# Kernel optimization log

Measured on AMD Instinct MI355X. Metric: run time of the kernel, lower is better.

## Reference

```python
import jax, jax.numpy as jnp
import numpy as np

B, L, H, NH, NB = 16, 256, 64, 2, 2
HS = H // NH
MAXLEN, TIME_SPAN, ITEMNUM = 256, 256, 50000
NEG = -4294967295.0  # -2**32 + 1
EPS = 1e-8


def layernorm(x, g, b):
    m = jnp.mean(x, axis=-1, keepdims=True)
    v = jnp.mean((x - m) ** 2, axis=-1, keepdims=True)
    return g * (x - m) / jnp.sqrt(v + EPS) + b


def setup_inputs() -> dict:
    key = jax.random.key(0)
    ks = jax.random.split(key, 24)
    s = 0.02
    inp = {
        "seqs_data": jax.random.randint(ks[0], (B, L), 0, ITEMNUM, dtype=jnp.int32),
        "seqs": jax.random.normal(ks[1], (B, L, H), dtype=jnp.float32),
        "positions": jax.random.randint(ks[2], (B, L), 0, MAXLEN, dtype=jnp.int32),
        "time_matrices": jax.random.randint(ks[3], (B, L, L), 0, TIME_SPAN + 1, dtype=jnp.int32),
        "abs_pos_K_tab": jax.random.normal(ks[4], (MAXLEN, H)) * s,
        "abs_pos_V_tab": jax.random.normal(ks[5], (MAXLEN, H)) * s,
        "time_K_tab": jax.random.normal(ks[6], (TIME_SPAN + 1, H)) * s,
        "time_V_tab": jax.random.normal(ks[7], (TIME_SPAN + 1, H)) * s,
        "Qw": jax.random.normal(ks[8], (NB, H, H)) * s,
        "Qb": jnp.zeros((NB, H)),
        "Kw": jax.random.normal(ks[9], (NB, H, H)) * s,
        "Kb": jnp.zeros((NB, H)),
        "Vw": jax.random.normal(ks[10], (NB, H, H)) * s,
        "Vb": jnp.zeros((NB, H)),
        "ln1_g": jnp.ones((NB, H)), "ln1_b": jnp.zeros((NB, H)),
        "ln2_g": jnp.ones((NB, H)), "ln2_b": jnp.zeros((NB, H)),
        "ffn_W1": jax.random.normal(ks[11], (NB, H, H)) * s,
        "ffn_b1": jnp.zeros((NB, H)),
        "ffn_W2": jax.random.normal(ks[12], (NB, H, H)) * s,
        "ffn_b2": jnp.zeros((NB, H)),
        "last_g": jnp.ones((H,)), "last_b": jnp.zeros((H,)),
    }
    return inp


def _forward(seqs_data, seqs, positions, time_matrices,
             abs_pos_K_tab, abs_pos_V_tab, time_K_tab, time_V_tab,
             Qw, Qb, Kw, Kb, Vw, Vb, ln1_g, ln1_b, ln2_g, ln2_b,
             ffn_W1, ffn_b1, ffn_W2, ffn_b2, last_g, last_b):
    # abs-pos embeddings with padding_idx=0 (zero row, no grad flow to it)
    pos_keep = (positions != 0)[..., None].astype(seqs.dtype)
    abs_pos_K = abs_pos_K_tab[positions] * pos_keep            # [B,L,H]
    abs_pos_V = abs_pos_V_tab[positions] * pos_keep
    time_K = time_K_tab[time_matrices]                         # [B,L,L,H]
    time_V = time_V_tab[time_matrices]
    tmK = time_K.reshape(B, L, L, NH, HS)
    tmV = time_V.reshape(B, L, L, NH, HS)
    aK = abs_pos_K.reshape(B, L, NH, HS)
    aV = abs_pos_V.reshape(B, L, NH, HS)

    timeline_mask = (seqs_data == ITEMNUM - 1)                 # [B,L] True = pad
    keep = (~timeline_mask)[..., None].astype(seqs.dtype)
    seqs = seqs * keep
    causal = ~jnp.tril(jnp.ones((L, L), dtype=bool))           # [L,L] upper tri
    full_mask = timeline_mask[:, None, :, None] | causal[None, None]  # [B,1,L,L]

    for i in range(NB):
        q_in = layernorm(seqs, ln1_g[i], ln1_b[i])
        Q = (q_in @ Qw[i].T + Qb[i]).reshape(B, L, NH, HS)
        K = (seqs @ Kw[i].T + Kb[i]).reshape(B, L, NH, HS)
        V = (seqs @ Vw[i].T + Vb[i]).reshape(B, L, NH, HS)
        aw = (jnp.einsum('blhd,bmhd->bhlm', Q, K)
              + jnp.einsum('blhd,bmhd->bhlm', Q, aK)
              + jnp.einsum('blmhd,blhd->bhlm', tmK, Q)) / (HS ** 0.5)
        aw = jnp.where(full_mask, NEG, aw)
        A = jax.nn.softmax(aw, axis=-1)                        # [B,NH,L,L]
        out = (jnp.einsum('bhlm,bmhd->blhd', A, V)
               + jnp.einsum('bhlm,bmhd->blhd', A, aV)
               + jnp.einsum('bhlm,blmhd->blhd', A, tmV)).reshape(B, L, H)
        seqs = q_in + out
        seqs = layernorm(seqs, ln2_g[i], ln2_b[i])
        h = jax.nn.relu(seqs @ ffn_W1[i].T + ffn_b1[i])
        seqs = (h @ ffn_W2[i].T + ffn_b2[i]) + seqs
        seqs = seqs * keep
    return layernorm(seqs, last_g, last_b)


def reference(seqs_data, seqs, positions, time_matrices,
              abs_pos_K_tab, abs_pos_V_tab, time_K_tab, time_V_tab,
              Qw, Qb, Kw, Kb, Vw, Vb, ln1_g, ln1_b, ln2_g, ln2_b,
              ffn_W1, ffn_b1, ffn_W2, ffn_b2, last_g, last_b):
    return _forward(seqs_data, seqs, positions, time_matrices,
                    abs_pos_K_tab, abs_pos_V_tab, time_K_tab, time_V_tab,
                    Qw, Qb, Kw, Kb, Vw, Vb, ln1_g, ln1_b, ln2_g, ln2_b,
                    ffn_W1, ffn_b1, ffn_W2, ffn_b2, last_g, last_b)
```

## Files before the change

### kernel.cpp

```cpp
#include <hip/hip_runtime.h>
#include <math.h>

#define BATCH 16
#define SEQL  256
#define HDIM  64
#define NBLK  2
#define PADID 49999
#define NEGV  -4294967295.0f
#define LNEPS 1e-8f
#define INV_SQRT_HS 0.17677669529663687f
#define TKC   257
#define TKTLD 260
#define QG    4

__device__ __forceinline__ float waveReduceSum(float v) {
#pragma unroll
    for (int o = 32; o > 0; o >>= 1) v += __shfl_xor(v, o);
    return v;
}

__global__ __launch_bounds__(256) void setup_kernel(
    const float* __restrict__ Qw, const float* __restrict__ Kw,
    const float* __restrict__ Vw, const float* __restrict__ W1,
    const float* __restrict__ W2, const float* __restrict__ tKtab,
    float* __restrict__ QwT, float* __restrict__ KwT, float* __restrict__ VwT,
    float* __restrict__ W1T, float* __restrict__ W2T, float* __restrict__ tKtabT)
{
    __shared__ float tile[64][65];
    const int tid = threadIdx.x;
    const int blk = blockIdx.x;
    if (blk < 10) {
        const float* srcs[10] = {Qw, Qw+4096, Kw, Kw+4096, Vw, Vw+4096,
                                 W1, W1+4096, W2, W2+4096};
        float*       dsts[10] = {QwT, QwT+4096, KwT, KwT+4096, VwT, VwT+4096,
                                 W1T, W1T+4096, W2T, W2T+4096};
        const float* s = srcs[blk];
        float*       d = dsts[blk];
        for (int p = 0; p < 16; ++p) {
            int r = p*4 + (tid>>6), c = tid&63;
            tile[r][c] = s[r*64 + c];
        }
        __syncthreads();
        for (int p = 0; p < 16; ++p) {
            int mth = p*4 + (tid>>6), t = tid&63;
            d[mth*64 + t] = tile[t][mth];
        }
    } else {
        const int s0 = (blk - 10) * 64;
        const int nrows = min(64, TKC - s0);
        for (int p = 0; p < 16; ++p) {
            int rr = p*4 + (tid>>6), c = tid&63;
            if (rr < nrows) tile[rr][c] = tKtab[(size_t)(s0+rr)*64 + c];
        }
        __syncthreads();
        for (int p = 0; p < 16; ++p) {
            int dd = p*4 + (tid>>6), cc = tid&63;
            if (cc < nrows) tKtabT[dd*TKTLD + s0 + cc] = tile[cc][dd];
        }
    }
}

__global__ __launch_bounds__(256) void prep_kernel(
    const float* __restrict__ xin, const int* __restrict__ seqs_data,
    const int* __restrict__ positions,
    const float* __restrict__ QwT, const float* __restrict__ Qb,
    const float* __restrict__ KwT, const float* __restrict__ Kb,
    const float* __restrict__ VwT, const float* __restrict__ Vb,
    const float* __restrict__ g1, const float* __restrict__ b1,
    const float* __restrict__ apK, const float* __restrict__ apV,
    float* __restrict__ q_in, float* __restrict__ Qo,
    float* __restrict__ KpT, float* __restrict__ Vp)
{
    const int w = threadIdx.x >> 6;
    const int t = threadIdx.x & 63;
    const int row0 = blockIdx.x * 4;
    const int row = row0 + w;
    float x = xin[(size_t)row * HDIM + t];
    if (seqs_data[row] == PADID) x = 0.f;

    float mean = waveReduceSum(x) * (1.f / HDIM);
    float d = x - mean;
    float var = waveReduceSum(d * d) * (1.f / HDIM);
    float q = g1[t] * d / sqrtf(var + LNEPS) + b1[t];

    __shared__ float xs[4][HDIM];
    __shared__ float qs[4][HDIM];
    __shared__ float kx[HDIM][5];
    xs[w][t] = x; qs[w][t] = q;
    q_in[(size_t)row * HDIM + t] = q;

    int pos = positions[row];
    float aK = pos ? apK[(size_t)pos * HDIM + t] : 0.f;
    float aV = pos ? apV[(size_t)pos * HDIM + t] : 0.f;

    float aq = 0.f, ak = 0.f, av = 0.f;
#pragma unroll 16
    for (int mth = 0; mth < 64; ++mth) {
        float qm = qs[w][mth], xm = xs[w][mth];
        aq += qm * QwT[mth*64 + t];
        ak += xm * KwT[mth*64 + t];
        av += xm * VwT[mth*64 + t];
    }
    Qo[(size_t)row * HDIM + t] = aq + Qb[t];
    Vp[(size_t)row * HDIM + t] = av + Vb[t] + aV;
    kx[t][w] = ak + Kb[t] + aK;
    __syncthreads();
    const int f = threadIdx.x >> 2, j = threadIdx.x & 3;
    KpT[(size_t)f * 4096 + row0 + j] = kx[f][j];
}

__global__ __launch_bounds__(512) void attn_kernel(
    const float* __restrict__ Qo, const float* __restrict__ KpT,
    const float* __restrict__ Vp, const float* __restrict__ q_in,
    const int* __restrict__ seqs_data, const int* __restrict__ tmat,
    const float* __restrict__ tVtab, const float* __restrict__ tKtabT,
    float* __restrict__ x2)
{
    const int hw  = blockIdx.x;
    const int blk = (hw & 7) * 128 + (hw >> 3);
    const int b   = blk >> 6;
    const int l0  = (blk & 63) << 2;
    const int row0 = b * SEQL + l0;
    const int tid = threadIdx.x;
    const int m   = tid & 255;
    const int h   = tid >> 8;
    const int lane = tid & 63;
    const int wv  = tid >> 6;
    const int mw  = wv & 3;

    __shared__ float qs_l[QG][HDIM];
    __shared__ float Tk_l[QG][2][TKTLD];
    __shared__ float A_s[QG][2][SEQL];
    __shared__ float Wl[QG][2][TKTLD];
    __shared__ float outred[8][QG][HDIM];
    __shared__ float redm[QG][2][4];
    __shared__ float reds[QG][2][4];

    for (int k = tid; k < QG*2*TKTLD; k += 512) ((float*)Wl)[k] = 0.f;
    if (tid < QG*HDIM)
        qs_l[tid >> 6][tid & 63] = Qo[(size_t)(row0 + (tid >> 6)) * HDIM + (tid & 63)];

    bool qpad[QG]; bool anypad = false;
#pragma unroll
    for (int li = 0; li < QG; ++li) {
        qpad[li] = (seqs_data[row0 + li] == PADID);
        anypad |= qpad[li];
    }
    const int lmax = l0 + QG - 1;
    int tmc[QG];
#pragma unroll
    for (int li = 0; li < QG; ++li)
        tmc[li] = tmat[(size_t)(row0 + li) * SEQL + m];
    __syncthreads();

    if (tid < TKC) {
        const int c = tid;
        float a00=0.f,a10=0.f,a20=0.f,a30=0.f, a01=0.f,a11=0.f,a21=0.f,a31=0.f;
#pragma unroll 8
        for (int dd = 0; dd < 32; ++dd) {
            float tt = tKtabT[dd*TKTLD + c];
            a00 += tt * qs_l[0][dd]; a10 += tt * qs_l[1][dd];
            a20 += tt * qs_l[2][dd]; a30 += tt * qs_l[3][dd];
        }
#pragma unroll 8
        for (int dd = 32; dd < 64; ++dd) {
            float tt = tKtabT[dd*TKTLD + c];
            a01 += tt * qs_l[0][dd]; a11 += tt * qs_l[1][dd];
            a21 += tt * qs_l[2][dd]; a31 += tt * qs_l[3][dd];
        }
        Tk_l[0][0][c]=a00; Tk_l[1][0][c]=a10; Tk_l[2][0][c]=a20; Tk_l[3][0][c]=a30;
        Tk_l[0][1][c]=a01; Tk_l[1][1][c]=a11; Tk_l[2][1][c]=a21; Tk_l[3][1][c]=a31;
    }
    __syncthreads();

    float sv[QG];
    const bool waveAllMasked = (mw * 64 > lmax) && !anypad;
    if (waveAllMasked) {
#pragma unroll
        for (int li = 0; li < QG; ++li) sv[li] = NEGV;
    } else {
        float s0=0.f, s1=0.f, s2=0.f, s3=0.f;
        const float* kpb = KpT + (size_t)(h*32) * 4096 + (size_t)b * SEQL + m;
        const float* q0 = &qs_l[0][h*32];
        const float* q1 = &qs_l[1][h*32];
        const float* q2 = &qs_l[2][h*32];
        const float* q3 = &qs_l[3][h*32];
#pragma unroll 8
        for (int dd = 0; dd < 32; ++dd) {
            float kv = kpb[(size_t)dd * 4096];
            s0 += kv * q0[dd]; s1 += kv * q1[dd];
            s2 += kv * q2[dd]; s3 += kv * q3[dd];
        }
        float sarr[QG] = {s0, s1, s2, s3};
#pragma unroll
        for (int li = 0; li < QG; ++li) {
            float s = (sarr[li] + Tk_l[li][h][tmc[li]]) * INV_SQRT_HS;
            const bool masked = (m > l0 + li) || qpad[li];
            sv[li] = masked ? NEGV : s;
        }
    }
#pragma unroll
    for (int li = 0; li < QG; ++li) {
        float a = sv[li];
#pragma unroll
        for (int o = 32; o > 0; o >>= 1) a = fmaxf(a, __shfl_xor(a, o));
        if (lane == 0) redm[li][h][mw] = a;
    }
    __syncthreads();
#pragma unroll
    for (int li = 0; li < QG; ++li) {
        float mx = fmaxf(fmaxf(redm[li][h][0], redm[li][h][1]),
                         fmaxf(redm[li][h][2], redm[li][h][3]));
        float e = __expf(sv[li] - mx);
        sv[li] = e;
        float t = waveReduceSum(e);
        if (lane == 0) reds[li][h][mw] = t;
    }
    __syncthreads();
#pragma unroll
    for (int li = 0; li < QG; ++li) {
        float sum = reds[li][h][0] + reds[li][h][1] + reds[li][h][2] + reds[li][h][3];
        float a = sv[li] / sum;
        A_s[li][h][m] = a;
        if (a != 0.f) atomicAdd(&Wl[li][h][tmc[li]], a);
    }
    __syncthreads();

    const int hd = tid & 63, chunk = tid >> 6;
    const int hh = hd >> 5;
    float acc0 = 0.f, acc1 = 0.f, acc2 = 0.f, acc3 = 0.f;

    const int mend = anypad ? SEQL : (lmax + 1 < SEQL ? lmax + 1 : SEQL);
    const float* vpb = Vp + (size_t)(b * SEQL) * HDIM + hd;
    int mm = chunk;
    for (; mm + 8 < mend; mm += 16) {
        float v0 = vpb[(size_t)(mm)   * HDIM];
        float v1 = vpb[(size_t)(mm+8) * HDIM];
        acc0 += A_s[0][hh][mm]*v0 + A_s[0][hh][mm+8]*v1;
        acc1 += A_s[1][hh][mm]*v0 + A_s[1][hh][mm+8]*v1;
        acc2 += A_s[2][hh][mm]*v0 + A_s[2][hh][mm+8]*v1;
        acc3 += A_s[3][hh][mm]*v0 + A_s[3][hh][mm+8]*v1;
    }
    for (; mm < mend; mm += 8) {
        float vp = vpb[(size_t)mm * HDIM];
        acc0 += A_s[0][hh][mm]*vp; acc1 += A_s[1][hh][mm]*vp;
        acc2 += A_s[2][hh][mm]*vp; acc3 += A_s[3][hh][mm]*vp;
    }
    const float* tvb = tVtab + hd;
    int c = chunk;
    for (; c + 8 < TKC; c += 16) {
        float t0 = tvb[(size_t)(c)   * HDIM];
        float t1 = tvb[(size_t)(c+8) * HDIM];
        acc0 += Wl[0][hh][c]*t0 + Wl[0][hh][c+8]*t1;
        acc1 += Wl[1][hh][c]*t0 + Wl[1][hh][c+8]*t1;
        acc2 += Wl[2][hh][c]*t0 + Wl[2][hh][c+8]*t1;
        acc3 += Wl[3][hh][c]*t0 + Wl[3][hh][c+8]*t1;
    }
    for (; c < TKC; c += 8) {
        float tv = tvb[(size_t)c * HDIM];
        acc0 += Wl[0][hh][c]*tv; acc1 += Wl[1][hh][c]*tv;
        acc2 += Wl[2][hh][c]*tv; acc3 += Wl[3][hh][c]*tv;
    }
    outred[chunk][0][hd] = acc0;
    outred[chunk][1][hd] = acc1;
    outred[chunk][2][hd] = acc2;
    outred[chunk][3][hd] = acc3;
    __syncthreads();
    if (tid < 256) {
        const int li = tid >> 6, dcol = tid & 63;
        const int row = row0 + li;
        float o = outred[0][li][dcol] + outred[1][li][dcol]
                + outred[2][li][dcol] + outred[3][li][dcol]
                + outred[4][li][dcol] + outred[5][li][dcol]
                + outred[6][li][dcol] + outred[7][li][dcol];
        x2[(size_t)row * HDIM + dcol] = q_in[(size_t)row * HDIM + dcol] + o;
    }
}

__global__ __launch_bounds__(256) void ffnprep_kernel(
    const float* __restrict__ x2, const int* __restrict__ seqs_data,
    const int* __restrict__ positions,
    const float* __restrict__ g2, const float* __restrict__ bg2,
    const float* __restrict__ W1T, const float* __restrict__ bb1,
    const float* __restrict__ W2T, const float* __restrict__ bb2,
    const float* __restrict__ g1n, const float* __restrict__ b1n,
    const float* __restrict__ QwT, const float* __restrict__ Qb,
    const float* __restrict__ KwT, const float* __restrict__ Kb,
    const float* __restrict__ VwT, const float* __restrict__ Vb,
    const float* __restrict__ apK, const float* __restrict__ apV,
    float* __restrict__ q_in, float* __restrict__ Qo,
    float* __restrict__ KpT, float* __restrict__ Vp)
{
    const int w = threadIdx.x >> 6;
    const int t = threadIdx.x & 63;
    const int row0 = blockIdx.x * 4;
    const int row = row0 + w;
    float x = x2[(size_t)row * HDIM + t];
    float mean = waveReduceSum(x) * (1.f / HDIM);
    float d = x - mean;
    float var = waveReduceSum(d * d) * (1.f / HDIM);
    float s = g2[t] * d / sqrtf(var + LNEPS) + bg2[t];

    __shared__ float ss[4][HDIM];
    __shared__ float hs[4][HDIM];
    __shared__ float kx[HDIM][5];
    ss[w][t] = s;
    float acc = 0.f;
#pragma unroll 16
    for (int mth = 0; mth < 64; ++mth)
        acc += ss[w][mth] * W1T[mth*64 + t];
    float hval = fmaxf(acc + bb1[t], 0.f);
    hs[w][t] = hval;
    float acc2 = 0.f;
#pragma unroll 16
    for (int mth = 0; mth < 64; ++mth)
        acc2 += hs[w][mth] * W2T[mth*64 + t];
    float y = acc2 + bb2[t] + s;
    if (seqs_data[row] == PADID) y = 0.f;

    float mean2 = waveReduceSum(y) * (1.f / HDIM);
    float d2 = y - mean2;
    float var2 = waveReduceSum(d2 * d2) * (1.f / HDIM);
    float q = g1n[t] * d2 / sqrtf(var2 + LNEPS) + b1n[t];

    ss[w][t] = y;
    hs[w][t] = q;
    q_in[(size_t)row * HDIM + t] = q;

    int pos = positions[row];
    float aK = pos ? apK[(size_t)pos * HDIM + t] : 0.f;
    float aV = pos ? apV[(size_t)pos * HDIM + t] : 0.f;

    float aq = 0.f, ak = 0.f, av = 0.f;
#pragma unroll 16
    for (int mth = 0; mth < 64; ++mth) {
        float qm = hs[w][mth], ym = ss[w][mth];
        aq += qm * QwT[mth*64 + t];
        ak += ym * KwT[mth*64 + t];
        av += ym * VwT[mth*64 + t];
    }
    Qo[(size_t)row * HDIM + t] = aq + Qb[t];
    Vp[(size_t)row * HDIM + t] = av + Vb[t] + aV;
    kx[t][w] = ak + Kb[t] + aK;
    __syncthreads();
    const int f = threadIdx.x >> 2, j = threadIdx.x & 3;
    KpT[(size_t)f * 4096 + row0 + j] = kx[f][j];
}

__global__ __launch_bounds__(256) void ffnfinal_kernel(
    const float* __restrict__ x2, const int* __restrict__ seqs_data,
    const float* __restrict__ g2, const float* __restrict__ bg2,
    const float* __restrict__ W1T, const float* __restrict__ bb1,
    const float* __restrict__ W2T, const float* __restrict__ bb2,
    const float* __restrict__ lg, const float* __restrict__ lb,
    float* __restrict__ dout)
{
    const int w = threadIdx.x >> 6;
    const int t = threadIdx.x & 63;
    const int row = blockIdx.x * 4 + w;
    float x = x2[(size_t)row * HDIM + t];
    float mean = waveReduceSum(x) * (1.f / HDIM);
    float d = x - mean;
    float var = waveReduceSum(d * d) * (1.f / HDIM);
    float s = g2[t] * d / sqrtf(var + LNEPS) + bg2[t];

    __shared__ float ss[4][HDIM];
    __shared__ float hs[4][HDIM];
    ss[w][t] = s;
    float acc = 0.f;
#pragma unroll 16
    for (int mth = 0; mth < 64; ++mth)
        acc += ss[w][mth] * W1T[mth*64 + t];
    float hval = fmaxf(acc + bb1[t], 0.f);
    hs[w][t] = hval;
    float acc2 = 0.f;
#pragma unroll 16
    for (int mth = 0; mth < 64; ++mth)
        acc2 += hs[w][mth] * W2T[mth*64 + t];
    float y = acc2 + bb2[t] + s;
    if (seqs_data[row] == PADID) y = 0.f;
    float m2 = waveReduceSum(y) * (1.f / HDIM);
    float dd = y - m2;
    float v2 = waveReduceSum(dd * dd) * (1.f / HDIM);
    dout[(size_t)row * HDIM + t] = lg[t] * dd / sqrtf(v2 + LNEPS) + lb[t];
}

extern "C" void kernel_launch(void* const* d_in, const int* in_sizes, int n_in,
                              void* d_out, int out_size, void* d_ws, size_t ws_size,
                              hipStream_t stream) {
    const int*   seqs_data = (const int*)d_in[0];
    const float* seqs      = (const float*)d_in[1];
    const int*   positions = (const int*)d_in[2];
    const int*   tmat      = (const int*)d_in[3];
    const float* apK       = (const float*)d_in[4];
    const float* apV       = (const float*)d_in[5];
    const float* tKtab     = (const float*)d_in[6];
    const float* tVtab     = (const float*)d_in[7];
    const float* Qw = (const float*)d_in[8];
    const float* Qb = (const float*)d_in[9];
    const float* Kw = (const float*)d_in[10];
    const float* Kb = (const float*)d_in[11];
    const float* Vw = (const float*)d_in[12];
    const float* Vb = (const float*)d_in[13];
    const float* g1 = (const float*)d_in[14];
    const float* b1 = (const float*)d_in[15];
    const float* g2 = (const float*)d_in[16];
    const float* b2 = (const float*)d_in[17];
    const float* W1 = (const float*)d_in[18];
    const float* fb1 = (const float*)d_in[19];
    const float* W2 = (const float*)d_in[20];
    const float* fb2 = (const float*)d_in[21];
    const float* lastg = (const float*)d_in[22];
    const float* lastb = (const float*)d_in[23];

    const size_t N = (size_t)BATCH * SEQL * HDIM;
    float* ws    = (float*)d_ws;
    float* x     = ws;
    float* q_in  = ws + 1 * N;
    float* Qo    = ws + 2 * N;
    float* Vp    = ws + 3 * N;
    float* KpT   = ws + 4 * N;
    float* wtbase = ws + 5 * N;
    float* QwT = wtbase;
    float* KwT = wtbase + 8192;
    float* VwT = wtbase + 16384;
    float* W1T = wtbase + 24576;
    float* W2T = wtbase + 32768;
    float* tKtabT = wtbase + 40960;

    const int rows = BATCH * SEQL;

    setup_kernel<<<15, 256, 0, stream>>>(Qw, Kw, Vw, W1, W2, tKtab,
                                         QwT, KwT, VwT, W1T, W2T, tKtabT);

    prep_kernel<<<rows / 4, 256, 0, stream>>>(
        seqs, seqs_data, positions,
        QwT, Qb, KwT, Kb, VwT, Vb, g1, b1,
        apK, apV, q_in, Qo, KpT, Vp);

    attn_kernel<<<rows / QG, 512, 0, stream>>>(
        Qo, KpT, Vp, q_in, seqs_data, tmat, tVtab, tKtabT, x);

    ffnprep_kernel<<<rows / 4, 256, 0, stream>>>(
        x, seqs_data, positions,
        g2, b2, W1T, fb1, W2T, fb2,
        g1 + HDIM, b1 + HDIM,
        QwT + 4096, Qb + HDIM, KwT + 4096, Kb + HDIM, VwT + 4096, Vb + HDIM,
        apK, apV, q_in, Qo, KpT, Vp);

    attn_kernel<<<rows / QG, 512, 0, stream>>>(
        Qo, KpT, Vp, q_in, seqs_data, tmat, tVtab, tKtabT, x);

    ffnfinal_kernel<<<rows / 4, 256, 0, stream>>>(
        x, seqs_data,
        g2 + HDIM, b2 + HDIM, W1T + 4096, fb1 + HDIM, W2T + 4096, fb2 + HDIM,
        lastg, lastb, (float*)d_out);
}
```

Before: 205.9 us.

## Split fused attention into score/softmax kernel and output aggregation kernel

The single attention kernel, which handled four query rows per 512-thread block, becomes two kernels. The first computes scores and softmax for two query rows per block and writes the probabilities and time-bucket weights to global memory. The second computes the A·V and time-value products with one wave per output row, reading the stored rows with float4 loads. This spreads work over more, smaller blocks and removes the cross-chunk shared-memory reduction, but adds a memset, an extra launch and a global round trip of about 8 MB per layer for A and Wg.

```diff
diff --git a/kernel.cpp b/kernel.cpp
--- a/kernel.cpp
+++ b/kernel.cpp
@@ -4,14 +4,14 @@
 #define BATCH 16
 #define SEQL  256
 #define HDIM  64
-#define NBLK  2
 #define PADID 49999
 #define NEGV  -4294967295.0f
 #define LNEPS 1e-8f
 #define INV_SQRT_HS 0.17677669529663687f
 #define TKC   257
 #define TKTLD 260
-#define QG    4
+#define WGLD  260
+#define ROWS  4096
 
 __device__ __forceinline__ float waveReduceSum(float v) {
 #pragma unroll
@@ -106,175 +106,158 @@
     kx[t][w] = ak + Kb[t] + aK;
     __syncthreads();
     const int f = threadIdx.x >> 2, j = threadIdx.x & 3;
-    KpT[(size_t)f * 4096 + row0 + j] = kx[f][j];
-}
-
-__global__ __launch_bounds__(512) void attn_kernel(
+    KpT[(size_t)f * ROWS + row0 + j] = kx[f][j];
+}
+
+__global__ __launch_bounds__(256) void attn_score_kernel(
     const float* __restrict__ Qo, const float* __restrict__ KpT,
-    const float* __restrict__ Vp, const float* __restrict__ q_in,
-    const int* __restrict__ seqs_data, const int* __restrict__ tmat,
-    const float* __restrict__ tVtab, const float* __restrict__ tKtabT,
-    float* __restrict__ x2)
-{
-    const int hw  = blockIdx.x;
-    const int blk = (hw & 7) * 128 + (hw >> 3);
-    const int b   = blk >> 6;
-    const int l0  = (blk & 63) << 2;
+    const float* __restrict__ tKtabT, const int* __restrict__ seqs_data,
+    const int* __restrict__ tmat, float* __restrict__ A, float* __restrict__ Wg)
+{
+    const int hw = blockIdx.x;
+    const int blk = ((hw & 7) << 8) | (hw >> 3);
+    const int b = blk >> 7, l0 = (blk & 127) << 1;
     const int row0 = b * SEQL + l0;
-    const int tid = threadIdx.x;
-    const int m   = tid & 255;
-    const int h   = tid >> 8;
-    const int lane = tid & 63;
-    const int wv  = tid >> 6;
-    const int mw  = wv & 3;
-
-    __shared__ float qs_l[QG][HDIM];
-    __shared__ float Tk_l[QG][2][TKTLD];
-    __shared__ float A_s[QG][2][SEQL];
-    __shared__ float Wl[QG][2][TKTLD];
-    __shared__ float outred[8][QG][HDIM];
-    __shared__ float redm[QG][2][4];
-    __shared__ float reds[QG][2][4];
-
-    for (int k = tid; k < QG*2*TKTLD; k += 512) ((float*)Wl)[k] = 0.f;
-    if (tid < QG*HDIM)
-        qs_l[tid >> 6][tid & 63] = Qo[(size_t)(row0 + (tid >> 6)) * HDIM + (tid & 63)];
-
-    bool qpad[QG]; bool anypad = false;
-#pragma unroll
-    for (int li = 0; li < QG; ++li) {
-        qpad[li] = (seqs_data[row0 + li] == PADID);
-        anypad |= qpad[li];
-    }
-    const int lmax = l0 + QG - 1;
-    int tmc[QG];
-#pragma unroll
-    for (int li = 0; li < QG; ++li)
-        tmc[li] = tmat[(size_t)(row0 + li) * SEQL + m];
-    __syncthreads();
-
-    if (tid < TKC) {
-        const int c = tid;
-        float a00=0.f,a10=0.f,a20=0.f,a30=0.f, a01=0.f,a11=0.f,a21=0.f,a31=0.f;
+    const int tid = threadIdx.x, m = tid, lane = tid & 63, wv = tid >> 6;
+
+    __shared__ float qs[2][HDIM];
+    __shared__ float Tk[2][2][TKTLD];
+    __shared__ float redm[2][2][4];
+    __shared__ float reds[2][2][4];
+
+    if (tid < 2*HDIM)
+        qs[tid >> 6][tid & 63] = Qo[(size_t)(row0 + (tid >> 6))*HDIM + (tid & 63)];
+    const bool qpad0 = (seqs_data[row0]     == PADID);
+    const bool qpad1 = (seqs_data[row0 + 1] == PADID);
+    const int tm0 = tmat[(size_t)row0*SEQL + m];
+    const int tm1 = tmat[(size_t)(row0+1)*SEQL + m];
+    __syncthreads();
+
+    for (int c = tid; c < TKC; c += 256) {
+        float a00=0.f,a01=0.f,a10=0.f,a11=0.f;
 #pragma unroll 8
         for (int dd = 0; dd < 32; ++dd) {
             float tt = tKtabT[dd*TKTLD + c];
-            a00 += tt * qs_l[0][dd]; a10 += tt * qs_l[1][dd];
-            a20 += tt * qs_l[2][dd]; a30 += tt * qs_l[3][dd];
+            a00 += tt*qs[0][dd]; a10 += tt*qs[1][dd];
         }
 #pragma unroll 8
         for (int dd = 32; dd < 64; ++dd) {
             float tt = tKtabT[dd*TKTLD + c];
-            a01 += tt * qs_l[0][dd]; a11 += tt * qs_l[1][dd];
-            a21 += tt * qs_l[2][dd]; a31 += tt * qs_l[3][dd];
-        }
-        Tk_l[0][0][c]=a00; Tk_l[1][0][c]=a10; Tk_l[2][0][c]=a20; Tk_l[3][0][c]=a30;
-        Tk_l[0][1][c]=a01; Tk_l[1][1][c]=a11; Tk_l[2][1][c]=a21; Tk_l[3][1][c]=a31;
-    }
-    __syncthreads();
-
-    float sv[QG];
-    const bool waveAllMasked = (mw * 64 > lmax) && !anypad;
+            a01 += tt*qs[0][dd]; a11 += tt*qs[1][dd];
+        }
+        Tk[0][0][c]=a00; Tk[0][1][c]=a01; Tk[1][0][c]=a10; Tk[1][1][c]=a11;
+    }
+    __syncthreads();
+
+    float s00, s01, s10, s11;
+    const bool anypad = qpad0 || qpad1;
+    const bool waveAllMasked = (wv*64 > l0 + 1) && !anypad;
     if (waveAllMasked) {
-#pragma unroll
-        for (int li = 0; li < QG; ++li) sv[li] = NEGV;
+        s00 = s01 = s10 = s11 = NEGV;
     } else {
-        float s0=0.f, s1=0.f, s2=0.f, s3=0.f;
-        const float* kpb = KpT + (size_t)(h*32) * 4096 + (size_t)b * SEQL + m;
-        const float* q0 = &qs_l[0][h*32];
-        const float* q1 = &qs_l[1][h*32];
-        const float* q2 = &qs_l[2][h*32];
-        const float* q3 = &qs_l[3][h*32];
+        float t00=0.f,t01=0.f,t10=0.f,t11=0.f;
+        const float* kpb = KpT + (size_t)b*SEQL + m;
 #pragma unroll 8
         for (int dd = 0; dd < 32; ++dd) {
-            float kv = kpb[(size_t)dd * 4096];
-            s0 += kv * q0[dd]; s1 += kv * q1[dd];
-            s2 += kv * q2[dd]; s3 += kv * q3[dd];
-        }
-        float sarr[QG] = {s0, s1, s2, s3};
+            float kv = kpb[(size_t)dd*ROWS];
+            t00 += kv*qs[0][dd]; t10 += kv*qs[1][dd];
+        }
+#pragma unroll 8
+        for (int dd = 32; dd < 64; ++dd) {
+            float kv = kpb[(size_t)dd*ROWS];
+            t01 += kv*qs[0][dd]; t11 += kv*qs[1][dd];
+        }
+        s00 = (t00 + Tk[0][0][tm0]) * INV_SQRT_HS;
+        s01 = (t01 + Tk[0][1][tm0]) * INV_SQRT_HS;
+        s10 = (t10 + Tk[1][0][tm1]) * INV_SQRT_HS;
+        s11 = (t11 + Tk[1][1][tm1]) * INV_SQRT_HS;
+        if ((m > l0)     || qpad0) { s00 = NEGV; s01 = NEGV; }
+        if ((m > l0 + 1) || qpad1) { s10 = NEGV; s11 = NEGV; }
+    }
+    {
+        float a0=s00, a1=s01, a2=s10, a3=s11;
 #pragma unroll
-        for (int li = 0; li < QG; ++li) {
-            float s = (sarr[li] + Tk_l[li][h][tmc[li]]) * INV_SQRT_HS;
-            const bool masked = (m > l0 + li) || qpad[li];
-            sv[li] = masked ? NEGV : s;
-        }
-    }
-#pragma unroll
-    for (int li = 0; li < QG; ++li) {
-        float a = sv[li];
-#pragma unroll
-        for (int o = 32; o > 0; o >>= 1) a = fmaxf(a, __shfl_xor(a, o));
-        if (lane == 0) redm[li][h][mw] = a;
-    }
-    __syncthreads();
-#pragma unroll
-    for (int li = 0; li < QG; ++li) {
-        float mx = fmaxf(fmaxf(redm[li][h][0], redm[li][h][1]),
-                         fmaxf(redm[li][h][2], redm[li][h][3]));
-        float e = __expf(sv[li] - mx);
-        sv[li] = e;
-        float t = waveReduceSum(e);
-        if (lane == 0) reds[li][h][mw] = t;
-    }
-    __syncthreads();
-#pragma unroll
-    for (int li = 0; li < QG; ++li) {
-        float sum = reds[li][h][0] + reds[li][h][1] + reds[li][h][2] + reds[li][h][3];
-        float a = sv[li] / sum;
-        A_s[li][h][m] = a;
-        if (a != 0.f) atomicAdd(&Wl[li][h][tmc[li]], a);
-    }
-    __syncthreads();
-
-    const int hd = tid & 63, chunk = tid >> 6;
-    const int hh = hd >> 5;
-    float acc0 = 0.f, acc1 = 0.f, acc2 = 0.f, acc3 = 0.f;
-
-    const int mend = anypad ? SEQL : (lmax + 1 < SEQL ? lmax + 1 : SEQL);
-    const float* vpb = Vp + (size_t)(b * SEQL) * HDIM + hd;
-    int mm = chunk;
-    for (; mm + 8 < mend; mm += 16) {
-        float v0 = vpb[(size_t)(mm)   * HDIM];
-        float v1 = vpb[(size_t)(mm+8) * HDIM];
-        acc0 += A_s[0][hh][mm]*v0 + A_s[0][hh][mm+8]*v1;
-        acc1 += A_s[1][hh][mm]*v0 + A_s[1][hh][mm+8]*v1;
-        acc2 += A_s[2][hh][mm]*v0 + A_s[2][hh][mm+8]*v1;
-        acc3 += A_s[3][hh][mm]*v0 + A_s[3][hh][mm+8]*v1;
-    }
-    for (; mm < mend; mm += 8) {
-        float vp = vpb[(size_t)mm * HDIM];
-        acc0 += A_s[0][hh][mm]*vp; acc1 += A_s[1][hh][mm]*vp;
-        acc2 += A_s[2][hh][mm]*vp; acc3 += A_s[3][hh][mm]*vp;
-    }
-    const float* tvb = tVtab + hd;
-    int c = chunk;
-    for (; c + 8 < TKC; c += 16) {
-        float t0 = tvb[(size_t)(c)   * HDIM];
-        float t1 = tvb[(size_t)(c+8) * HDIM];
-        acc0 += Wl[0][hh][c]*t0 + Wl[0][hh][c+8]*t1;
-        acc1 += Wl[1][hh][c]*t0 + Wl[1][hh][c+8]*t1;
-        acc2 += Wl[2][hh][c]*t0 + Wl[2][hh][c+8]*t1;
-        acc3 += Wl[3][hh][c]*t0 + Wl[3][hh][c+8]*t1;
-    }
-    for (; c < TKC; c += 8) {
-        float tv = tvb[(size_t)c * HDIM];
-        acc0 += Wl[0][hh][c]*tv; acc1 += Wl[1][hh][c]*tv;
-        acc2 += Wl[2][hh][c]*tv; acc3 += Wl[3][hh][c]*tv;
-    }
-    outred[chunk][0][hd] = acc0;
-    outred[chunk][1][hd] = acc1;
-    outred[chunk][2][hd] = acc2;
-    outred[chunk][3][hd] = acc3;
-    __syncthreads();
-    if (tid < 256) {
-        const int li = tid >> 6, dcol = tid & 63;
-        const int row = row0 + li;
-        float o = outred[0][li][dcol] + outred[1][li][dcol]
-                + outred[2][li][dcol] + outred[3][li][dcol]
-                + outred[4][li][dcol] + outred[5][li][dcol]
-                + outred[6][li][dcol] + outred[7][li][dcol];
-        x2[(size_t)row * HDIM + dcol] = q_in[(size_t)row * HDIM + dcol] + o;
-    }
+        for (int o = 32; o > 0; o >>= 1) {
+            a0 = fmaxf(a0, __shfl_xor(a0, o));
+            a1 = fmaxf(a1, __shfl_xor(a1, o));
+            a2 = fmaxf(a2, __shfl_xor(a2, o));
+            a3 = fmaxf(a3, __shfl_xor(a3, o));
+        }
+        if (lane == 0) {
+            redm[0][0][wv]=a0; redm[0][1][wv]=a1; redm[1][0][wv]=a2; redm[1][1][wv]=a3;
+        }
+    }
+    __syncthreads();
+    float M00 = fmaxf(fmaxf(redm[0][0][0],redm[0][0][1]), fmaxf(redm[0][0][2],redm[0][0][3]));
+    float M01 = fmaxf(fmaxf(redm[0][1][0],redm[0][1][1]), fmaxf(redm[0][1][2],redm[0][1][3]));
+    float M10 = fmaxf(fmaxf(redm[1][0][0],redm[1][0][1]), fmaxf(redm[1][0][2],redm[1][0][3]));
+    float M11 = fmaxf(fmaxf(redm[1][1][0],redm[1][1][1]), fmaxf(redm[1][1][2],redm[1][1][3]));
+    float e00 = __expf(s00 - M00), e01 = __expf(s01 - M01);
+    float e10 = __expf(s10 - M10), e11 = __expf(s11 - M11);
+    {
+        float t0 = waveReduceSum(e00), t1 = waveReduceSum(e01);
+        float t2 = waveReduceSum(e10), t3 = waveReduceSum(e11);
+        if (lane == 0) {
+            reds[0][0][wv]=t0; reds[0][1][wv]=t1; reds[1][0][wv]=t2; reds[1][1][wv]=t3;
+        }
+    }
+    __syncthreads();
+    float S00 = reds[0][0][0]+reds[0][0][1]+reds[0][0][2]+reds[0][0][3];
+    float S01 = reds[0][1][0]+reds[0][1][1]+reds[0][1][2]+reds[0][1][3];
+    float S10 = reds[1][0][0]+reds[1][0][1]+reds[1][0][2]+reds[1][0][3];
+    float S11 = reds[1][1][0]+reds[1][1][1]+reds[1][1][2]+reds[1][1][3];
+    float r00 = e00/S00, r01 = e01/S01, r10 = e10/S10, r11 = e11/S11;
+    A[((size_t)row0*2 + 0)*SEQL + m]     = r00;
+    A[((size_t)row0*2 + 1)*SEQL + m]     = r01;
+    A[((size_t)(row0+1)*2 + 0)*SEQL + m] = r10;
+    A[((size_t)(row0+1)*2 + 1)*SEQL + m] = r11;
+    if (r00 != 0.f) atomicAdd(&Wg[((size_t)row0*2 + 0)*WGLD + tm0], r00);
+    if (r01 != 0.f) atomicAdd(&Wg[((size_t)row0*2 + 1)*WGLD + tm0], r01);
+    if (r10 != 0.f) atomicAdd(&Wg[((size_t)(row0+1)*2 + 0)*WGLD + tm1], r10);
+    if (r11 != 0.f) atomicAdd(&Wg[((size_t)(row0+1)*2 + 1)*WGLD + tm1], r11);
+}
+
+__global__ __launch_bounds__(256) void attn_out_kernel(
+    const float* __restrict__ A, const float* __restrict__ Wg,
+    const float* __restrict__ Vp, const float* __restrict__ tVtab,
+    const float* __restrict__ q_in, const int* __restrict__ seqs_data,
+    float* __restrict__ x2)
+{
+    const int hw = blockIdx.x;
+    const int blk = ((hw & 7) << 7) | (hw >> 3);
+    const int row = (blk << 2) + (threadIdx.x >> 6);
+    const int t = threadIdx.x & 63;
+    const int h = t >> 5;
+    const int b = row >> 8, l = row & 255;
+    const bool qpad = (seqs_data[row] == PADID);
+    const int mend = qpad ? SEQL : l + 1;
+
+    const float4* arow4 = (const float4*)(A + ((size_t)row*2 + h)*SEQL);
+    const float*  arow  = (const float*)arow4;
+    const float*  vpb   = Vp + (size_t)(b*SEQL)*HDIM + t;
+    float acc = 0.f;
+    int mm = 0;
+    for (; mm + 3 < mend; mm += 4) {
+        float4 a4 = arow4[mm >> 2];
+        float v0 = vpb[(size_t)(mm)  *HDIM];
+        float v1 = vpb[(size_t)(mm+1)*HDIM];
+        float v2 = vpb[(size_t)(mm+2)*HDIM];
+        float v3 = vpb[(size_t)(mm+3)*HDIM];
+        acc += a4.x*v0 + a4.y*v1 + a4.z*v2 + a4.w*v3;
+    }
+    for (; mm < mend; ++mm) acc += arow[mm] * vpb[(size_t)mm*HDIM];
+
+    const float4* wrow4 = (const float4*)(Wg + ((size_t)row*2 + h)*WGLD);
+    const float*  tvb   = tVtab + t;
+#pragma unroll 4
+    for (int c = 0; c < 256; c += 4) {
+        float4 w4 = wrow4[c >> 2];
+        acc += w4.x*tvb[(size_t)(c)  *HDIM] + w4.y*tvb[(size_t)(c+1)*HDIM]
+             + w4.z*tvb[(size_t)(c+2)*HDIM] + w4.w*tvb[(size_t)(c+3)*HDIM];
+    }
+    acc += ((const float*)wrow4)[256] * tvb[(size_t)256*HDIM];
+
+    x2[(size_t)row*HDIM + t] = q_in[(size_t)row*HDIM + t] + acc;
 }
 
 __global__ __launch_bounds__(256) void ffnprep_kernel(
@@ -344,7 +327,7 @@
     kx[t][w] = ak + Kb[t] + aK;
     __syncthreads();
     const int f = threadIdx.x >> 2, j = threadIdx.x & 3;
-    KpT[(size_t)f * 4096 + row0 + j] = kx[f][j];
+    KpT[(size_t)f * ROWS + row0 + j] = kx[f][j];
 }
 
 __global__ __launch_bounds__(256) void ffnfinal_kernel(
@@ -413,7 +396,7 @@
     const float* lastg = (const float*)d_in[22];
     const float* lastb = (const float*)d_in[23];
 
-    const size_t N = (size_t)BATCH * SEQL * HDIM;
+    const size_t N = (size_t)ROWS * HDIM;
     float* ws    = (float*)d_ws;
     float* x     = ws;
     float* q_in  = ws + 1 * N;
@@ -427,8 +410,11 @@
     float* W1T = wtbase + 24576;
     float* W2T = wtbase + 32768;
     float* tKtabT = wtbase + 40960;
-
-    const int rows = BATCH * SEQL;
+    float* A   = wtbase + 40960 + 64*TKTLD;
+    float* Wg  = A + (size_t)ROWS * 2 * SEQL;
+    const size_t WgBytes = (size_t)ROWS * 2 * WGLD * sizeof(float);
+
+    const int rows = ROWS;
 
     setup_kernel<<<15, 256, 0, stream>>>(Qw, Kw, Vw, W1, W2, tKtab,
                                          QwT, KwT, VwT, W1T, W2T, tKtabT);
@@ -438,8 +424,11 @@
         QwT, Qb, KwT, Kb, VwT, Vb, g1, b1,
         apK, apV, q_in, Qo, KpT, Vp);
 
-    attn_kernel<<<rows / QG, 512, 0, stream>>>(
-        Qo, KpT, Vp, q_in, seqs_data, tmat, tVtab, tKtabT, x);
+    hipMemsetAsync(Wg, 0, WgBytes, stream);
+    attn_score_kernel<<<rows / 2, 256, 0, stream>>>(
+        Qo, KpT, tKtabT, seqs_data, tmat, A, Wg);
+    attn_out_kernel<<<rows / 4, 256, 0, stream>>>(
+        A, Wg, Vp, tVtab, q_in, seqs_data, x);
 
     ffnprep_kernel<<<rows / 4, 256, 0, stream>>>(
         x, seqs_data, positions,
@@ -448,8 +437,11 @@
         QwT + 4096, Qb + HDIM, KwT + 4096, Kb + HDIM, VwT + 4096, Vb + HDIM,
         apK, apV, q_in, Qo, KpT, Vp);
 
-    attn_kernel<<<rows / QG, 512, 0, stream>>>(
-        Qo, KpT, Vp, q_in, seqs_data, tmat, tVtab, tKtabT, x);
+    hipMemsetAsync(Wg, 0, WgBytes, stream);
+    attn_score_kernel<<<rows / 2, 256, 0, stream>>>(
+        Qo, KpT, tKtabT, seqs_data, tmat, A, Wg);
+    attn_out_kernel<<<rows / 4, 256, 0, stream>>>(
+        A, Wg, Vp, tVtab, q_in, seqs_data, x);
 
     ffnfinal_kernel<<<rows / 4, 256, 0, stream>>>(
         x, seqs_data,
```

Result: slower. 286.4 us (+39.1%).
